# Performance work log

Hardware: AMD Instinct MI355X
Metric: run time of the kernel (lower is better)

Reference implementation:

```python
import jax, jax.numpy as jnp
import numpy as np
from jax import lax

TERNARY_THRESHOLD = 0.001


def ternary_quantize(w):
    # clamp to [-1,1], then threshold to {-1, 0, 1}
    wc = jnp.clip(w, -1.0, 1.0)
    return jnp.where(wc > TERNARY_THRESHOLD, 1.0,
                     jnp.where(wc < -TERNARY_THRESHOLD, -1.0, 0.0))


def setup_inputs() -> dict:
    key = jax.random.key(0)
    k1, k2, k3, k4, k5 = jax.random.split(key, 5)
    B, C, H, W = 16, 256, 64, 64
    x = jax.random.normal(k1, (B, C, H, W), dtype=jnp.float32)
    time_emb = jax.random.normal(k2, (B, 4 * C), dtype=jnp.float32)
    y = jax.random.randint(k3, (B,), 0, 1000)
    # conv params (OIHW); small scale so ternary quantization yields a mix of {-1,0,1}
    weight = jax.random.normal(k4, (C, C, 3, 3), dtype=jnp.float32) * 0.02
    bias = jax.random.normal(k5, (C,), dtype=jnp.float32) * 0.01
    return {"x": x, "time_emb": time_emb, "y": y, "weight": weight, "bias": bias}


def reference(x, time_emb, y, weight, bias):
    up = jnp.repeat(jnp.repeat(x, 2, axis=2), 2, axis=3)
    # ternary quantize weights (STE identity grad via stop_gradient residual)
    qw = weight + lax.stop_gradient(ternary_quantize(weight) - weight)
    out = lax.conv_general_dilated(
        up, qw,
        window_strides=(1, 1),
        padding=((1, 1), (1, 1)),
        dimension_numbers=("NCHW", "OIHW", "NCHW"),
    )
    return out + bias[None, :, None, None]
```

## Files before the change

### kernel.cpp

```cpp
#include <hip/hip_runtime.h>
#include <hip/hip_bf16.h>


using i8x16 = __attribute__((ext_vector_type(16))) char;
using i32x4 = __attribute__((ext_vector_type(4))) int;
using f32x2 = __attribute__((ext_vector_type(2))) float;

#define MFMAI8(a, b, c) __builtin_amdgcn_mfma_i32_16x16x64_i8(a, b, c, 0, 0, 0)

#define QSCALE 0.044881889763779525f
#define QINV   22.280701754385966f

static __device__ __forceinline__ void gload_lds16(const void* g, void* l) {
  __builtin_amdgcn_global_load_lds(
      (const __attribute__((address_space(1))) unsigned int*)g,
      (__attribute__((address_space(3))) unsigned int*)l, 16, 0, 0);
}

__global__ void prep_xpose_kernel(const float* __restrict__ x,
                                  char* __restrict__ xT,
                                  const float* __restrict__ w,
                                  char* __restrict__ wq) {
  __shared__ float tile[64][65];
  int bidx = blockIdx.x;
  if (bidx < 4096) {
    int cb = bidx & 3, h = (bidx >> 2) & 63, b = bidx >> 8;
    int t = threadIdx.x;
    int ci_l = t >> 2, wseg = (t & 3) * 16;
    const float* src = x + ((size_t)((b * 256 + cb * 64 + ci_l) * 64 + h) * 64 + wseg);
#pragma unroll
    for (int j = 0; j < 16; ++j) tile[ci_l][wseg + j] = src[j];
    __syncthreads();
    int w_l = t >> 2, seg = t & 3;
    i8x16 o;
#pragma unroll
    for (int j = 0; j < 16; ++j) {
      int qv = (int)rintf(tile[seg * 16 + j][w_l] * QINV);
      qv = qv > 127 ? 127 : (qv < -127 ? -127 : qv);
      o[j] = (char)qv;
    }
    char* dst = xT + ((size_t)((b * 64 + h) * 64 + w_l)) * 256 + cb * 64 + seg * 16;
    *(i8x16*)dst = o;
  } else {
    int t = (bidx - 4096) * 256 + threadIdx.x;
    int co = t >> 8, ci = t & 255;
    const float* wp = w + (size_t)(co * 256 + ci) * 9;
    int q[3][3];
#pragma unroll
    for (int kh = 0; kh < 3; ++kh)
#pragma unroll
      for (int kw = 0; kw < 3; ++kw) {
        float xv = wp[kh * 3 + kw];
        q[kh][kw] = (xv > 0.001f) ? 1 : ((xv < -0.001f) ? -1 : 0);
      }
    int wid = co >> 5, fm = (co >> 4) & 1;
    int u = ci >> 6;
    int lane = (co & 15) | (((ci >> 4) & 3) << 4);
    int e = ci & 15;
#pragma unroll
    for (int pa = 0; pa < 2; ++pa)
#pragma unroll
      for (int pb = 0; pb < 2; ++pb)
#pragma unroll
        for (int dh = 0; dh < 2; ++dh)
#pragma unroll
          for (int dw = 0; dw < 2; ++dw) {
            int h0 = dh * (1 + pa), h1 = dh ? 3 : (1 + pa);
            int w0 = dw * (1 + pb), w1 = dw ? 3 : (1 + pb);
            int s = 0;
            for (int kh = h0; kh < h1; ++kh)
              for (int kw = w0; kw < w1; ++kw) s += q[kh][kw];
            size_t idx = (size_t)(pa * 2 + dh) * 262144 + (size_t)wid * 32768 +
                         (size_t)u * 8192 + (size_t)(pb * 4 + dw * 2 + fm) * 1024 +
                         lane * 16 + e;
            wq[idx] = (char)s;
          }
  }
}

__launch_bounds__(512, 2)
__global__ void conv_kernel(const char* __restrict__ xT,
                            const char* __restrict__ wq,
                            const float* __restrict__ bias,
                            float* __restrict__ out) {
  __shared__ __align__(16) unsigned char Bs[2 * 16384];

  int bid = blockIdx.x;
  int idx = (bid & 7) * 256 + (bid >> 3);
  int pa = idx & 1;
  int h  = (idx >> 1) & 63;
  int bb = idx >> 7;

  int t = threadIdx.x;
  int lane = t & 63, wid = t >> 6;
  int lr = lane & 15, l4 = lane >> 4;

  bool dhok0 = (h - 1 + pa) >= 0;
  bool dhok1 = (h + pa) <= 63;

  int colS = (t >> 2) & 63;
  int segL = (t & 3) ^ ((colS >> 1) & 3);
  const char* gb = xT + (size_t)bb * 64 * 64 * 256;
  int gof0 = colS * 256 + (t >> 8) * 64 + segL * 16;
  unsigned char* lw = Bs + wid * 1024;

  if (dhok0) {
    const char* rowb = gb + (size_t)(h - 1 + pa) * 16384;
    gload_lds16(rowb + gof0, lw);
    gload_lds16(rowb + gof0 + 128, lw + 8192);
  } else {
    const i8x16 z = (i8x16)0;
    *(i8x16*)(Bs + t * 16) = z;
    *(i8x16*)(Bs + 8192 + t * 16) = z;
  }

  int colb[3][4], sego[3];
#pragma unroll
  for (int s3 = 0; s3 < 3; ++s3) {
    int v = lr + s3 - 1;
    sego[s3] = ((l4 ^ ((v >> 1) & 3)) << 4);
#pragma unroll
    for (int fn = 0; fn < 4; ++fn)
      colb[s3][fn] = (((fn * 16 + v) & 63) << 6);
  }
  bool zlo = (lr == 0);
  bool zhi = (lr == 15);
  const i32x4 zfr = {0, 0, 0, 0};

  i32x4 acc[2][2][4];
#pragma unroll
  for (int p = 0; p < 2; ++p)
#pragma unroll
    for (int m = 0; m < 2; ++m)
#pragma unroll
      for (int n = 0; n < 4; ++n) acc[p][m][n] = (i32x4){0, 0, 0, 0};

  const char* awave = wq + (size_t)((pa * 2) * 8 + wid) * 32768 + lane * 16;

  __syncthreads();

  if (dhok1) {
    const char* rowb = gb + (size_t)(h + pa) * 16384;
    gload_lds16(rowb + gof0, lw + 16384);
    gload_lds16(rowb + gof0 + 128, lw + 16384 + 8192);
  } else {
    const i8x16 z = (i8x16)0;
    *(i8x16*)(Bs + 16384 + t * 16) = z;
    *(i8x16*)(Bs + 16384 + 8192 + t * 16) = z;
  }

#define UNIT(ADH, BDH, U)                                                     \
  do {                                                                        \
    const char* au = (ADH) + (U) * 8192;                                      \
    i32x4 a0 = *(const i32x4*)(au);                                           \
    i32x4 a1 = *(const i32x4*)(au + 1024);                                    \
    i32x4 a2 = *(const i32x4*)(au + 2048);                                    \
    i32x4 a3 = *(const i32x4*)(au + 3072);                                    \
    i32x4 a4 = *(const i32x4*)(au + 4096);                                    \
    i32x4 a5 = *(const i32x4*)(au + 5120);                                    \
    i32x4 a6 = *(const i32x4*)(au + 6144);                                    \
    i32x4 a7 = *(const i32x4*)(au + 7168);                                    \
    const unsigned char* bc = (BDH) + (U) * 4096;                             \
    i32x4 bf[4];                                                              \
    __builtin_amdgcn_s_setprio(1);                                            \
    _Pragma("unroll")                                                         \
    for (int fn = 0; fn < 4; ++fn)                                            \
      bf[fn] = *(const i32x4*)(bc + colb[0][fn] + sego[0]);                   \
    if (zlo) bf[0] = zfr;                                                     \
    _Pragma("unroll")                                                         \
    for (int fn = 0; fn < 4; ++fn) {                                          \
      acc[0][0][fn] = MFMAI8(a0, bf[fn], acc[0][0][fn]);                      \
      acc[0][1][fn] = MFMAI8(a1, bf[fn], acc[0][1][fn]);                      \
    }                                                                         \
    _Pragma("unroll")                                                         \
    for (int fn = 0; fn < 4; ++fn)                                            \
      bf[fn] = *(const i32x4*)(bc + colb[1][fn] + sego[1]);                   \
    _Pragma("unroll")                                                         \
    for (int fn = 0; fn < 4; ++fn) {                                          \
      acc[0][0][fn] = MFMAI8(a2, bf[fn], acc[0][0][fn]);                      \
      acc[0][1][fn] = MFMAI8(a3, bf[fn], acc[0][1][fn]);                      \
      acc[1][0][fn] = MFMAI8(a4, bf[fn], acc[1][0][fn]);                      \
      acc[1][1][fn] = MFMAI8(a5, bf[fn], acc[1][1][fn]);                      \
    }                                                                         \
    _Pragma("unroll")                                                         \
    for (int fn = 0; fn < 4; ++fn)                                            \
      bf[fn] = *(const i32x4*)(bc + colb[2][fn] + sego[2]);                   \
    if (zhi) bf[3] = zfr;                                                     \
    _Pragma("unroll")                                                         \
    for (int fn = 0; fn < 4; ++fn) {                                          \
      acc[1][0][fn] = MFMAI8(a6, bf[fn], acc[1][0][fn]);                      \
      acc[1][1][fn] = MFMAI8(a7, bf[fn], acc[1][1][fn]);                      \
    }                                                                         \
    __builtin_amdgcn_s_setprio(0);                                            \
  } while (0)

  if (dhok0) {
    const char* adh = awave;
    const unsigned char* bdh = Bs;
    UNIT(adh, bdh, 0);
    UNIT(adh, bdh, 1);
    UNIT(adh, bdh, 2);
    UNIT(adh, bdh, 3);
  }

  __syncthreads();

  if (dhok1) {
    const char* adh = awave + 262144;
    const unsigned char* bdh = Bs + 16384;
    UNIT(adh, bdh, 0);
    UNIT(adh, bdh, 1);
    UNIT(adh, bdh, 2);
    UNIT(adh, bdh, 3);
  }
#undef UNIT

  int oh = 2 * h + pa;
#pragma unroll
  for (int fm = 0; fm < 2; ++fm) {
    int co0 = wid * 32 + fm * 16 + l4 * 4;
#pragma unroll
    for (int i = 0; i < 4; ++i) {
      float bi = bias[co0 + i];
      float* orow = out + ((size_t)(bb * 256 + co0 + i) * 128 + oh) * 128;
#pragma unroll
      for (int fn = 0; fn < 4; ++fn) {
        int ww = fn * 16 + lr;
        f32x2 v = {fmaf(QSCALE, (float)acc[0][fm][fn][i], bi),
                   fmaf(QSCALE, (float)acc[1][fm][fn][i], bi)};
        __builtin_nontemporal_store(v, (f32x2*)(orow + 2 * ww));
      }
    }
  }
}

__global__ void fallback_kernel(const float* __restrict__ x,
                                const float* __restrict__ w,
                                const float* __restrict__ bias,
                                float* __restrict__ out, long total) {
  long i = (long)blockIdx.x * 256 + threadIdx.x;
  if (i >= total) return;
  int ow = i & 127; int oh = (int)((i >> 7) & 127);
  int co = (int)((i >> 14) & 255); int bb = (int)(i >> 22);
  float s = bias[co];
  for (int ci = 0; ci < 256; ++ci) {
    for (int kh = 0; kh < 3; ++kh) {
      int r = oh - 1 + kh;
      if (r < 0 || r > 127) continue;
      for (int kw = 0; kw < 3; ++kw) {
        int c = ow - 1 + kw;
        if (c < 0 || c > 127) continue;
        float wv = w[((co * 256 + ci) * 3 + kh) * 3 + kw];
        float q = (wv > 0.001f) ? 1.f : ((wv < -0.001f) ? -1.f : 0.f);
        s += q * x[((size_t)(bb * 256 + ci) * 64 + (r >> 1)) * 64 + (c >> 1)];
      }
    }
  }
  out[i] = s;
}

extern "C" void kernel_launch(void* const* d_in, const int* in_sizes, int n_in,
                              void* d_out, int out_size, void* d_ws, size_t ws_size,
                              hipStream_t stream) {
  const float* x    = (const float*)d_in[0];
  const float* wt   = (const float*)d_in[3];
  const float* bias = (const float*)d_in[4];
  float* out = (float*)d_out;

  size_t need = (size_t)18 * 1024 * 1024;
  if (ws_size < need) {
    long total = 67108864;
    fallback_kernel<<<(int)((total + 255) / 256), 256, 0, stream>>>(x, wt, bias, out, total);
    return;
  }
  char* wq = (char*)d_ws;
  char* xT = (char*)d_ws + 2 * 1024 * 1024;

  prep_xpose_kernel<<<4352, 256, 0, stream>>>(x, xT, wt, wq);
  conv_kernel<<<2048, 512, 0, stream>>>(xT, wq, bias, out);
}
```

Before: 91.18 us.

## Split conv blocks across output-channel halves with 256-thread blocks

Measured after the change: 89.87 us, median of 2. No clear change (-1.4%).

```diff
diff --git a/kernel.cpp b/kernel.cpp
--- a/kernel.cpp
+++ b/kernel.cpp
@@ -53,7 +53,7 @@
         float xv = wp[kh * 3 + kw];
         q[kh][kw] = (xv > 0.001f) ? 1 : ((xv < -0.001f) ? -1 : 0);
       }
-    int wid = co >> 5, fm = (co >> 4) & 1;
+    int wid8 = co >> 5, fm = (co >> 4) & 1;
     int u = ci >> 6;
     int lane = (co & 15) | (((ci >> 4) & 3) << 4);
     int e = ci & 15;
@@ -70,7 +70,7 @@
             int s = 0;
             for (int kh = h0; kh < h1; ++kh)
               for (int kw = w0; kw < w1; ++kw) s += q[kh][kw];
-            size_t idx = (size_t)(pa * 2 + dh) * 262144 + (size_t)wid * 32768 +
+            size_t idx = (size_t)(pa * 2 + dh) * 262144 + (size_t)wid8 * 32768 +
                          (size_t)u * 8192 + (size_t)(pb * 4 + dw * 2 + fm) * 1024 +
                          lane * 16 + e;
             wq[idx] = (char)s;
@@ -78,7 +78,7 @@
   }
 }
 
-__launch_bounds__(512, 2)
+__launch_bounds__(256, 2)
 __global__ void conv_kernel(const char* __restrict__ xT,
                             const char* __restrict__ wq,
                             const float* __restrict__ bias,
@@ -86,10 +86,11 @@
   __shared__ __align__(16) unsigned char Bs[2 * 16384];
 
   int bid = blockIdx.x;
-  int idx = (bid & 7) * 256 + (bid >> 3);
-  int pa = idx & 1;
-  int h  = (idx >> 1) & 63;
-  int bb = idx >> 7;
+  int idx = (bid & 7) * 512 + (bid >> 3);
+  int co_t = idx & 1;
+  int pa = (idx >> 1) & 1;
+  int h  = (idx >> 2) & 63;
+  int bb = idx >> 8;
 
   int t = threadIdx.x;
   int lane = t & 63, wid = t >> 6;
@@ -98,21 +99,29 @@
   bool dhok0 = (h - 1 + pa) >= 0;
   bool dhok1 = (h + pa) <= 63;
 
-  int colS = (t >> 2) & 63;
+  int colS = t >> 2;
   int segL = (t & 3) ^ ((colS >> 1) & 3);
-  const char* gb = xT + (size_t)bb * 64 * 64 * 256;
-  int gof0 = colS * 256 + (t >> 8) * 64 + segL * 16;
+  const char* gb = xT + (size_t)bb * 64 * 16384;
+  int gof0 = colS * 256 + segL * 16;
   unsigned char* lw = Bs + wid * 1024;
 
-  if (dhok0) {
-    const char* rowb = gb + (size_t)(h - 1 + pa) * 16384;
-    gload_lds16(rowb + gof0, lw);
-    gload_lds16(rowb + gof0 + 128, lw + 8192);
-  } else {
-    const i8x16 z = (i8x16)0;
-    *(i8x16*)(Bs + t * 16) = z;
-    *(i8x16*)(Bs + 8192 + t * 16) = z;
-  }
+#define STAGE(ROW, SLOT)                                                      \
+  do {                                                                        \
+    const char* rowb_ = gb + (size_t)(ROW) * 16384;                           \
+    _Pragma("unroll")                                                         \
+    for (int u_ = 0; u_ < 4; ++u_)                                            \
+      gload_lds16(rowb_ + gof0 + u_ * 64, lw + (SLOT) * 16384 + u_ * 4096);   \
+  } while (0)
+
+#define ZFILL(SLOT)                                                           \
+  do {                                                                        \
+    const i8x16 z_ = (i8x16)0;                                                \
+    _Pragma("unroll")                                                         \
+    for (int j_ = 0; j_ < 4; ++j_)                                            \
+      *(i8x16*)(Bs + (SLOT) * 16384 + t * 64 + j_ * 16) = z_;                 \
+  } while (0)
+
+  if (dhok0) STAGE(h - 1 + pa, 0); else ZFILL(0);
 
   int colb[3][4], sego[3];
 #pragma unroll
@@ -135,19 +144,12 @@
 #pragma unroll
       for (int n = 0; n < 4; ++n) acc[p][m][n] = (i32x4){0, 0, 0, 0};
 
-  const char* awave = wq + (size_t)((pa * 2) * 8 + wid) * 32768 + lane * 16;
+  const char* awave =
+      wq + (size_t)((pa * 2) * 8 + co_t * 4 + wid) * 32768 + lane * 16;
 
   __syncthreads();
 
-  if (dhok1) {
-    const char* rowb = gb + (size_t)(h + pa) * 16384;
-    gload_lds16(rowb + gof0, lw + 16384);
-    gload_lds16(rowb + gof0 + 128, lw + 16384 + 8192);
-  } else {
-    const i8x16 z = (i8x16)0;
-    *(i8x16*)(Bs + 16384 + t * 16) = z;
-    *(i8x16*)(Bs + 16384 + 8192 + t * 16) = z;
-  }
+  if (dhok1) STAGE(h + pa, 1); else ZFILL(1);
 
 #define UNIT(ADH, BDH, U)                                                     \
   do {                                                                        \
@@ -214,11 +216,13 @@
     UNIT(adh, bdh, 3);
   }
 #undef UNIT
+#undef STAGE
+#undef ZFILL
 
   int oh = 2 * h + pa;
 #pragma unroll
   for (int fm = 0; fm < 2; ++fm) {
-    int co0 = wid * 32 + fm * 16 + l4 * 4;
+    int co0 = (co_t * 4 + wid) * 32 + fm * 16 + l4 * 4;
 #pragma unroll
     for (int i = 0; i < 4; ++i) {
       float bi = bias[co0 + i];
@@ -277,5 +281,5 @@
   char* xT = (char*)d_ws + 2 * 1024 * 1024;
 
   prep_xpose_kernel<<<4352, 256, 0, stream>>>(x, xT, wt, wq);
-  conv_kernel<<<2048, 512, 0, stream>>>(xT, wq, bias, out);
-}
+  conv_kernel<<<4096, 256, 0, stream>>>(xT, wq, bias, out);
+}
```
